# Optimization experiments

Hardware: AMD Instinct MI355X
Metric: run time of the kernel (lower is better)

Reference implementation:

```python
import jax, jax.numpy as jnp
import numpy as np

N, IN_DIM, OUT_DIM = 8192, 256, 64
NEG_BIG = -9e15
LRELU_SLOPE = 0.01  # torch F.leaky_relu default


def setup_inputs() -> dict:
    key = jax.random.key(0)
    k1, k2, k3, k4 = jax.random.split(key, 4)
    inp = jax.random.normal(k1, (N, IN_DIM), dtype=jnp.float32)
    adj = jax.random.randint(k2, (N, N), 0, 2, dtype=jnp.int32)
    # xavier_uniform with gain=1.414
    limW = 1.414 * np.sqrt(6.0 / (IN_DIM + OUT_DIM))
    W = jax.random.uniform(k3, (IN_DIM, OUT_DIM), minval=-limW, maxval=limW, dtype=jnp.float32)
    lima = 1.414 * np.sqrt(6.0 / (2 * OUT_DIM + 1))
    a = jax.random.uniform(k4, (2 * OUT_DIM, 1), minval=-lima, maxval=lima, dtype=jnp.float32)
    return {"input": inp, "adj": adj, "W": W, "a": a}


def reference(input, adj, W, a):
    h = input @ W                      # [N, D]
    a1, a2 = a[:OUT_DIM, 0], a[OUT_DIM:, 0]
    # e[i,j] = leaky_relu(a1.h_i + a2.h_j) == the concat-based score, no NxNx2D tensor
    f1 = h @ a1                        # [N]
    f2 = h @ a2                        # [N]
    e = jax.nn.leaky_relu(f1[:, None] + f2[None, :], negative_slope=LRELU_SLOPE)  # [N, N]
    face_Rhand = e[1, 2]
    face_Lhand = e[1, 3]
    Rhand_Lhand = e[3, 2]
    attention = jnp.where(adj > 0, e, jnp.float32(NEG_BIG))
    alpha = jax.nn.softmax(attention, axis=1)
    h_prime = alpha @ h                # [N, D]
    return (h_prime, face_Rhand, face_Lhand, Rhand_Lhand)
```

## Files before the change

kernel.cpp:

```cpp
#include <hip/hip_runtime.h>
#include <hip/hip_bf16.h>

#define GN 8192
#define KD 256
#define OD 64
#define LOG2E 1.44269504f

typedef __attribute__((ext_vector_type(8))) short bf16x8;
typedef __attribute__((ext_vector_type(4))) float f32x4;

__device__ __forceinline__ float fexp2(float x) {
#if __has_builtin(__builtin_amdgcn_exp2f)
  return __builtin_amdgcn_exp2f(x);
#else
  return exp2f(x);
#endif
}

#if __has_builtin(__builtin_amdgcn_sched_barrier)
#define SCHED_FENCE() __builtin_amdgcn_sched_barrier(0)
#else
#define SCHED_FENCE()
#endif

__global__ __launch_bounds__(256) void gat_k1(
    const float* __restrict__ input, const float* __restrict__ W,
    const float* __restrict__ a, __hip_bfloat16* __restrict__ hT,
    float* __restrict__ f1p, float* __restrict__ f2p, float* __restrict__ out)
{
  __shared__ float Wl[KD * OD];
  __shared__ float inT[KD * 33];
  __shared__ float red1[8][32];
  __shared__ float red2[8][32];
  __shared__ float s1row[32];
  __shared__ float s2row[32];

  const int tid = threadIdx.x;
  const int i0 = blockIdx.x * 32;

  for (int idx = tid; idx < KD * OD / 4; idx += 256)
    ((float4*)Wl)[idx] = ((const float4*)W)[idx];

#pragma unroll
  for (int it = 0; it < 8; ++it) {
    int idx = tid + it * 256;
    int r = idx >> 6, k4 = idx & 63;
    float4 v = *(const float4*)(input + (long)(i0 + r) * KD + k4 * 4);
    inT[(k4 * 4 + 0) * 33 + r] = v.x;
    inT[(k4 * 4 + 1) * 33 + r] = v.y;
    inT[(k4 * 4 + 2) * 33 + r] = v.z;
    inT[(k4 * 4 + 3) * 33 + r] = v.w;
  }
  __syncthreads();

  const int r = tid & 31;
  const int cg = tid >> 5;
  float acc[8];
#pragma unroll
  for (int c = 0; c < 8; ++c) acc[c] = 0.f;

#pragma unroll 4
  for (int k = 0; k < KD; ++k) {
    float inv = inT[k * 33 + r];
    float4 wa = *(const float4*)&Wl[k * 64 + cg * 8];
    float4 wb = *(const float4*)&Wl[k * 64 + cg * 8 + 4];
    acc[0] += inv * wa.x; acc[1] += inv * wa.y;
    acc[2] += inv * wa.z; acc[3] += inv * wa.w;
    acc[4] += inv * wb.x; acc[5] += inv * wb.y;
    acc[6] += inv * wb.z; acc[7] += inv * wb.w;
  }

#pragma unroll
  for (int c = 0; c < 8; ++c)
    hT[(long)(cg * 8 + c) * GN + i0 + r] = __float2bfloat16(acc[c]);

  float s1 = 0.f, s2 = 0.f;
#pragma unroll
  for (int c = 0; c < 8; ++c) {
    s1 += acc[c] * a[cg * 8 + c];
    s2 += acc[c] * a[OD + cg * 8 + c];
  }
  red1[cg][r] = s1; red2[cg][r] = s2;
  __syncthreads();
  if (tid < 32) {
    float f1 = 0.f, f2 = 0.f;
#pragma unroll
    for (int g = 0; g < 8; ++g) { f1 += red1[g][tid]; f2 += red2[g][tid]; }
    s1row[tid] = f1; s2row[tid] = f2;
    f1p[i0 + tid] = f1 * LOG2E;
    f2p[i0 + tid] = f2 * LOG2E;
  }
  __syncthreads();
  if (blockIdx.x == 0 && tid == 0) {
    float e12 = s1row[1] + s2row[2];
    float e13 = s1row[1] + s2row[3];
    float e32 = s1row[3] + s2row[2];
    out[(long)GN * OD + 0] = fmaxf(e12, 0.01f * e12);
    out[(long)GN * OD + 1] = fmaxf(e13, 0.01f * e13);
    out[(long)GN * OD + 2] = fmaxf(e32, 0.01f * e32);
  }
}

struct Asl { int4 a0, a1; };
struct Bsl { bf16x8 b0, b1, b2, b3; };

__global__ __launch_bounds__(256, 2) void gat_k2(
    const int* __restrict__ adj, const __hip_bfloat16* __restrict__ hT,
    const float* __restrict__ f1p, const float* __restrict__ f2p,
    float* __restrict__ out)
{
  __shared__ float f2l[GN];

  const int tid = threadIdx.x;
  const int lane = tid & 63;
  const int wv = tid >> 6;
  const int tn = lane & 15;
  const int quad = lane >> 4;
  const int i0 = blockIdx.x * 16;
  const int jq = wv * 2048;

  for (int i = tid; i < GN / 4; i += 256)
    ((float4*)f2l)[i] = ((const float4*)f2p)[i];

  const float f1r = f1p[i0 + tn];
  __syncthreads();

  const int* ap = adj + (long)(i0 + tn) * GN + jq + quad * 8;
  const __hip_bfloat16* hp = hT + (long)tn * GN + jq + quad * 8;
  const float* f2q = f2l + jq + quad * 8;

  f32x4 acc[4];
#pragma unroll
  for (int nf = 0; nf < 4; ++nf) acc[nf] = (f32x4){0.f, 0.f, 0.f, 0.f};
  f32x4 accS = (f32x4){0.f, 0.f, 0.f, 0.f};

  bf16x8 ones;
  {
    short ov = (tn == 0) ? (short)0x3F80 : (short)0;
#pragma unroll
    for (int i = 0; i < 8; ++i) ones[i] = ov;
  }

  auto loadA = [&](int s) {
    Asl r;
    r.a0 = *(const int4*)(ap + s * 32);
    r.a1 = *(const int4*)(ap + s * 32 + 4);
    return r;
  };
  auto loadB = [&](int s) {
    Bsl r;
    r.b0 = *(const bf16x8*)(hp + 0 * 16 * (long)GN + s * 32);
    r.b1 = *(const bf16x8*)(hp + 1 * 16 * (long)GN + s * 32);
    r.b2 = *(const bf16x8*)(hp + 2 * 16 * (long)GN + s * 32);
    r.b3 = *(const bf16x8*)(hp + 3 * 16 * (long)GN + s * 32);
    return r;
  };
  auto computeSlice = [&](int s, const Asl& ca, const Bsl& cb) {
    const float4 f20 = *(const float4*)(f2q + s * 32);
    const float4 f21 = *(const float4*)(f2q + s * 32 + 4);
    float e0 = f1r + f20.x, e1 = f1r + f20.y, e2 = f1r + f20.z, e3 = f1r + f20.w;
    float e4 = f1r + f21.x, e5 = f1r + f21.y, e6 = f1r + f21.z, e7 = f1r + f21.w;
    float v0 = fexp2((ca.a0.x > 0) ? fmaxf(e0, 0.01f * e0) : -256.f);
    float v1 = fexp2((ca.a0.y > 0) ? fmaxf(e1, 0.01f * e1) : -256.f);
    float v2 = fexp2((ca.a0.z > 0) ? fmaxf(e2, 0.01f * e2) : -256.f);
    float v3 = fexp2((ca.a0.w > 0) ? fmaxf(e3, 0.01f * e3) : -256.f);
    float v4 = fexp2((ca.a1.x > 0) ? fmaxf(e4, 0.01f * e4) : -256.f);
    float v5 = fexp2((ca.a1.y > 0) ? fmaxf(e5, 0.01f * e5) : -256.f);
    float v6 = fexp2((ca.a1.z > 0) ? fmaxf(e6, 0.01f * e6) : -256.f);
    float v7 = fexp2((ca.a1.w > 0) ? fmaxf(e7, 0.01f * e7) : -256.f);
    union { bf16x8 v; unsigned u[4]; } wf;
    wf.u[0] = __builtin_amdgcn_perm(__float_as_uint(v1), __float_as_uint(v0), 0x07060302u);
    wf.u[1] = __builtin_amdgcn_perm(__float_as_uint(v3), __float_as_uint(v2), 0x07060302u);
    wf.u[2] = __builtin_amdgcn_perm(__float_as_uint(v5), __float_as_uint(v4), 0x07060302u);
    wf.u[3] = __builtin_amdgcn_perm(__float_as_uint(v7), __float_as_uint(v6), 0x07060302u);
    acc[0] = __builtin_amdgcn_mfma_f32_16x16x32_bf16(wf.v, cb.b0, acc[0], 0, 0, 0);
    acc[1] = __builtin_amdgcn_mfma_f32_16x16x32_bf16(wf.v, cb.b1, acc[1], 0, 0, 0);
    acc[2] = __builtin_amdgcn_mfma_f32_16x16x32_bf16(wf.v, cb.b2, acc[2], 0, 0, 0);
    acc[3] = __builtin_amdgcn_mfma_f32_16x16x32_bf16(wf.v, cb.b3, acc[3], 0, 0, 0);
    accS   = __builtin_amdgcn_mfma_f32_16x16x32_bf16(wf.v, ones,  accS,   0, 0, 0);
  };

  Asl A0 = loadA(0), A1 = loadA(1), A2 = loadA(2), A3 = loadA(3);
  Bsl B0 = loadB(0), B1 = loadB(1), B2 = loadB(2), B3 = loadB(3);
  SCHED_FENCE();

  for (int t = 0; t < 16; ++t) {
    const int s = t * 4;
    {
      Asl ca = A0; Bsl cb = B0;
      if (s + 4 < 64) { A0 = loadA(s + 4); B0 = loadB(s + 4); }
      SCHED_FENCE();
      computeSlice(s, ca, cb);
    }
    {
      Asl ca = A1; Bsl cb = B1;
      if (s + 5 < 64) { A1 = loadA(s + 5); B1 = loadB(s + 5); }
      SCHED_FENCE();
      computeSlice(s + 1, ca, cb);
    }
    {
      Asl ca = A2; Bsl cb = B2;
      if (s + 6 < 64) { A2 = loadA(s + 6); B2 = loadB(s + 6); }
      SCHED_FENCE();
      computeSlice(s + 2, ca, cb);
    }
    {
      Asl ca = A3; Bsl cb = B3;
      if (s + 7 < 64) { A3 = loadA(s + 7); B3 = loadB(s + 7); }
      SCHED_FENCE();
      computeSlice(s + 3, ca, cb);
    }
  }

  __syncthreads();
  float* pb = f2l;
  float* sb = f2l + 4 * 16 * 68;
#pragma unroll
  for (int nf = 0; nf < 4; ++nf)
#pragma unroll
    for (int rgi = 0; rgi < 4; ++rgi)
      pb[(wv * 16 + quad * 4 + rgi) * 68 + nf * 16 + tn] = acc[nf][rgi];
  if (tn == 0) {
#pragma unroll
    for (int rgi = 0; rgi < 4; ++rgi)
      sb[wv * 16 + quad * 4 + rgi] = accS[rgi];
  }
  __syncthreads();
  for (int t = tid; t < 16 * OD; t += 256) {
    int rr = t >> 6, cc = t & 63;
    float num = pb[(0 * 16 + rr) * 68 + cc] + pb[(1 * 16 + rr) * 68 + cc] +
                pb[(2 * 16 + rr) * 68 + cc] + pb[(3 * 16 + rr) * 68 + cc];
    float den = sb[0 * 16 + rr] + sb[1 * 16 + rr] + sb[2 * 16 + rr] + sb[3 * 16 + rr];
    out[(long)(i0 + rr) * OD + cc] = num / den;
  }
}

extern "C" void kernel_launch(void* const* d_in, const int* in_sizes, int n_in,
                              void* d_out, int out_size, void* d_ws, size_t ws_size,
                              hipStream_t stream) {
  const float* input = (const float*)d_in[0];
  const int* adj     = (const int*)d_in[1];
  const float* W     = (const float*)d_in[2];
  const float* a     = (const float*)d_in[3];
  float* out = (float*)d_out;

  char* ws = (char*)d_ws;
  __hip_bfloat16* hT = (__hip_bfloat16*)ws;
  float* f1p = (float*)(ws + (size_t)OD * GN * 2);
  float* f2p = f1p + GN;

  gat_k1<<<256, 256, 0, stream>>>(input, W, a, hT, f1p, f2p, out);
  gat_k2<<<512, 256, 0, stream>>>(adj, hT, f1p, f2p, out);
}
```

Baseline: 425.2 us.

## Pre-pack adjacency into bitmask and stream mask through LDS in attention kernel

Adds a kernel that converts the int32 adjacency matrix into a 64-bit ballot bitmask in one pure streaming pass. The attention/aggregation kernel then reads 1 bit per edge from LDS instead of 32-bit adjacency values from global memory, and masks by zeroing the exponent instead of using exp2(-256). With less register pressure it simplifies pipelining to double-buffered B loads and raises occupancy to 3 blocks. The full adjacency read remains but is moved into a separate bandwidth-bound launch; it adds an extra kernel launch and a workspace buffer.

```diff
diff --git a/kernel.cpp b/kernel.cpp
--- a/kernel.cpp
+++ b/kernel.cpp
@@ -5,6 +5,7 @@
 #define KD 256
 #define OD 64
 #define LOG2E 1.44269504f
+#define MSTR 257
 
 typedef __attribute__((ext_vector_type(8))) short bf16x8;
 typedef __attribute__((ext_vector_type(4))) float f32x4;
@@ -17,11 +18,18 @@
 #endif
 }
 
-#if __has_builtin(__builtin_amdgcn_sched_barrier)
-#define SCHED_FENCE() __builtin_amdgcn_sched_barrier(0)
-#else
-#define SCHED_FENCE()
-#endif
+__global__ __launch_bounds__(256) void gat_k0(
+    const int* __restrict__ adj, unsigned long long* __restrict__ mask)
+{
+  const long stride = (long)gridDim.x * 256;
+  long t = (long)blockIdx.x * 256 + threadIdx.x;
+  const int lane = threadIdx.x & 63;
+#pragma unroll 4
+  for (int it = 0; it < 64; ++it, t += stride) {
+    unsigned long long m = __ballot(adj[t] > 0);
+    if (lane == 0) mask[t >> 6] = m;
+  }
+}
 
 __global__ __launch_bounds__(256) void gat_k1(
     const float* __restrict__ input, const float* __restrict__ W,
@@ -101,15 +109,13 @@
   }
 }
 
-struct Asl { int4 a0, a1; };
-struct Bsl { bf16x8 b0, b1, b2, b3; };
-
-__global__ __launch_bounds__(256, 2) void gat_k2(
-    const int* __restrict__ adj, const __hip_bfloat16* __restrict__ hT,
+__global__ __launch_bounds__(256, 3) void gat_k2(
+    const unsigned* __restrict__ maskG, const __hip_bfloat16* __restrict__ hT,
     const float* __restrict__ f1p, const float* __restrict__ f2p,
     float* __restrict__ out)
 {
   __shared__ float f2l[GN];
+  __shared__ unsigned maskL[16 * MSTR];
 
   const int tid = threadIdx.x;
   const int lane = tid & 63;
@@ -117,17 +123,23 @@
   const int tn = lane & 15;
   const int quad = lane >> 4;
   const int i0 = blockIdx.x * 16;
-  const int jq = wv * 2048;
 
   for (int i = tid; i < GN / 4; i += 256)
     ((float4*)f2l)[i] = ((const float4*)f2p)[i];
+#pragma unroll
+  for (int it = 0; it < 16; ++it) {
+    int idx = tid + it * 256;
+    int r = idx >> 8, w = idx & 255;
+    maskL[r * MSTR + w] = maskG[(long)(i0 + r) * 256 + w];
+  }
 
   const float f1r = f1p[i0 + tn];
   __syncthreads();
 
-  const int* ap = adj + (long)(i0 + tn) * GN + jq + quad * 8;
+  const int jq = wv * 2048;
   const __hip_bfloat16* hp = hT + (long)tn * GN + jq + quad * 8;
   const float* f2q = f2l + jq + quad * 8;
+  const int mbase = tn * MSTR + wv * 64;
 
   f32x4 acc[4];
 #pragma unroll
@@ -141,12 +153,7 @@
     for (int i = 0; i < 8; ++i) ones[i] = ov;
   }
 
-  auto loadA = [&](int s) {
-    Asl r;
-    r.a0 = *(const int4*)(ap + s * 32);
-    r.a1 = *(const int4*)(ap + s * 32 + 4);
-    return r;
-  };
+  struct Bsl { bf16x8 b0, b1, b2, b3; };
   auto loadB = [&](int s) {
     Bsl r;
     r.b0 = *(const bf16x8*)(hp + 0 * 16 * (long)GN + s * 32);
@@ -155,61 +162,49 @@
     r.b3 = *(const bf16x8*)(hp + 3 * 16 * (long)GN + s * 32);
     return r;
   };
-  auto computeSlice = [&](int s, const Asl& ca, const Bsl& cb) {
+
+  Bsl Bb[2];
+  Bb[0] = loadB(0);
+  Bb[1] = loadB(1);
+
+  for (int s = 0; s < 64; ++s) {
+    Bsl cb = Bb[s & 1];
+    if (s + 2 < 64) Bb[s & 1] = loadB(s + 2);
+
+    const unsigned bits = (maskL[mbase + s] >> (quad * 8)) & 0xffu;
     const float4 f20 = *(const float4*)(f2q + s * 32);
     const float4 f21 = *(const float4*)(f2q + s * 32 + 4);
+
     float e0 = f1r + f20.x, e1 = f1r + f20.y, e2 = f1r + f20.z, e3 = f1r + f20.w;
     float e4 = f1r + f21.x, e5 = f1r + f21.y, e6 = f1r + f21.z, e7 = f1r + f21.w;
-    float v0 = fexp2((ca.a0.x > 0) ? fmaxf(e0, 0.01f * e0) : -256.f);
-    float v1 = fexp2((ca.a0.y > 0) ? fmaxf(e1, 0.01f * e1) : -256.f);
-    float v2 = fexp2((ca.a0.z > 0) ? fmaxf(e2, 0.01f * e2) : -256.f);
-    float v3 = fexp2((ca.a0.w > 0) ? fmaxf(e3, 0.01f * e3) : -256.f);
-    float v4 = fexp2((ca.a1.x > 0) ? fmaxf(e4, 0.01f * e4) : -256.f);
-    float v5 = fexp2((ca.a1.y > 0) ? fmaxf(e5, 0.01f * e5) : -256.f);
-    float v6 = fexp2((ca.a1.z > 0) ? fmaxf(e6, 0.01f * e6) : -256.f);
-    float v7 = fexp2((ca.a1.w > 0) ? fmaxf(e7, 0.01f * e7) : -256.f);
+    float v0 = fexp2(fmaxf(e0, 0.01f * e0));
+    float v1 = fexp2(fmaxf(e1, 0.01f * e1));
+    float v2 = fexp2(fmaxf(e2, 0.01f * e2));
+    float v3 = fexp2(fmaxf(e3, 0.01f * e3));
+    float v4 = fexp2(fmaxf(e4, 0.01f * e4));
+    float v5 = fexp2(fmaxf(e5, 0.01f * e5));
+    float v6 = fexp2(fmaxf(e6, 0.01f * e6));
+    float v7 = fexp2(fmaxf(e7, 0.01f * e7));
+    v0 = (bits & 1u)   ? v0 : 0.f;
+    v1 = (bits & 2u)   ? v1 : 0.f;
+    v2 = (bits & 4u)   ? v2 : 0.f;
+    v3 = (bits & 8u)   ? v3 : 0.f;
+    v4 = (bits & 16u)  ? v4 : 0.f;
+    v5 = (bits & 32u)  ? v5 : 0.f;
+    v6 = (bits & 64u)  ? v6 : 0.f;
+    v7 = (bits & 128u) ? v7 : 0.f;
+
     union { bf16x8 v; unsigned u[4]; } wf;
     wf.u[0] = __builtin_amdgcn_perm(__float_as_uint(v1), __float_as_uint(v0), 0x07060302u);
     wf.u[1] = __builtin_amdgcn_perm(__float_as_uint(v3), __float_as_uint(v2), 0x07060302u);
     wf.u[2] = __builtin_amdgcn_perm(__float_as_uint(v5), __float_as_uint(v4), 0x07060302u);
     wf.u[3] = __builtin_amdgcn_perm(__float_as_uint(v7), __float_as_uint(v6), 0x07060302u);
+
     acc[0] = __builtin_amdgcn_mfma_f32_16x16x32_bf16(wf.v, cb.b0, acc[0], 0, 0, 0);
     acc[1] = __builtin_amdgcn_mfma_f32_16x16x32_bf16(wf.v, cb.b1, acc[1], 0, 0, 0);
     acc[2] = __builtin_amdgcn_mfma_f32_16x16x32_bf16(wf.v, cb.b2, acc[2], 0, 0, 0);
     acc[3] = __builtin_amdgcn_mfma_f32_16x16x32_bf16(wf.v, cb.b3, acc[3], 0, 0, 0);
     accS   = __builtin_amdgcn_mfma_f32_16x16x32_bf16(wf.v, ones,  accS,   0, 0, 0);
-  };
-
-  Asl A0 = loadA(0), A1 = loadA(1), A2 = loadA(2), A3 = loadA(3);
-  Bsl B0 = loadB(0), B1 = loadB(1), B2 = loadB(2), B3 = loadB(3);
-  SCHED_FENCE();
-
-  for (int t = 0; t < 16; ++t) {
-    const int s = t * 4;
-    {
-      Asl ca = A0; Bsl cb = B0;
-      if (s + 4 < 64) { A0 = loadA(s + 4); B0 = loadB(s + 4); }
-      SCHED_FENCE();
-      computeSlice(s, ca, cb);
-    }
-    {
-      Asl ca = A1; Bsl cb = B1;
-      if (s + 5 < 64) { A1 = loadA(s + 5); B1 = loadB(s + 5); }
-      SCHED_FENCE();
-      computeSlice(s + 1, ca, cb);
-    }
-    {
-      Asl ca = A2; Bsl cb = B2;
-      if (s + 6 < 64) { A2 = loadA(s + 6); B2 = loadB(s + 6); }
-      SCHED_FENCE();
-      computeSlice(s + 2, ca, cb);
-    }
-    {
-      Asl ca = A3; Bsl cb = B3;
-      if (s + 7 < 64) { A3 = loadA(s + 7); B3 = loadB(s + 7); }
-      SCHED_FENCE();
-      computeSlice(s + 3, ca, cb);
-    }
   }
 
   __syncthreads();
@@ -248,7 +243,9 @@
   __hip_bfloat16* hT = (__hip_bfloat16*)ws;
   float* f1p = (float*)(ws + (size_t)OD * GN * 2);
   float* f2p = f1p + GN;
-
+  unsigned long long* mask = (unsigned long long*)(f2p + GN);
+
+  gat_k0<<<4096, 256, 0, stream>>>(adj, mask);
   gat_k1<<<256, 256, 0, stream>>>(input, W, a, hT, f1p, f2p, out);
-  gat_k2<<<512, 256, 0, stream>>>(adj, hT, f1p, f2p, out);
-}
+  gat_k2<<<512, 256, 0, stream>>>((const unsigned*)mask, hT, f1p, f2p, out);
+}
```

New measurement: 566.8 us. 1.33x slower.
